# Kernel optimization log

Measured on AMD Instinct MI355X. Metric: run time of the kernel, lower is better.

The kernel has to match this reference:

```python
import jax, jax.numpy as jnp
import numpy as np

B, C1, C2, NH, HC, EC, GC, NTXT, H, W = 8, 128, 128, 4, 32, 128, 512, 32, 160, 160
GA_HEADS, GA_HD, K_NN, NUM_SELECT = 4, 32, 6, 64  # graph attn: min(nh,4) heads, head_dim=C1/4
BN_EPS = 1e-5


def setup_inputs() -> dict:
    key = jax.random.key(0)
    ks = jax.random.split(key, 16)
    rn = lambda k, shape, s=0.05: jax.random.normal(k, shape, dtype=jnp.float32) * s
    return {
        'x': jax.random.normal(ks[0], (B, C1, H, W), dtype=jnp.float32),
        'guide': jax.random.normal(ks[1], (B, NTXT, GC), dtype=jnp.float32),
        'w_gm1': rn(ks[2], (C1 // 4, C1)), 'b_gm1': jnp.zeros((C1 // 4,), jnp.float32),
        'w_gm2': rn(ks[3], (GA_HEADS, C1 // 4)), 'b_gm2': jnp.zeros((GA_HEADS,), jnp.float32),
        'w_qkv': rn(ks[4], (3 * C1, C1)),
        'w_ge1': rn(ks[5], (C1 // 2, C1)), 'b_ge1': jnp.zeros((C1 // 2,), jnp.float32),
        'w_ge2': rn(ks[6], (GA_HEADS, C1 // 2)), 'b_ge2': jnp.zeros((GA_HEADS,), jnp.float32),
        'w_gl': rn(ks[7], (EC, GC)), 'b_gl': jnp.zeros((EC,), jnp.float32),
        'attn_bias': rn(ks[8], (NH,), 0.1),
        'w_proj': rn(ks[9], (C2, C1, 3, 3)),
        'bn_gamma': jnp.ones((C2,), jnp.float32), 'bn_beta': jnp.zeros((C2,), jnp.float32),
        'bn_mean': rn(ks[10], (C2,)),
        'bn_var': jax.random.uniform(ks[11], (C2,), jnp.float32, 0.5, 1.5),
    }


def _graph_attention(x, w_gm1, b_gm1, w_gm2, b_gm2, w_qkv, w_ge1, b_ge1, w_ge2, b_ge2):
    # EfficientGraphModulatedAttention.forward (eval mode, dropout off)
    b, c, h, w = x.shape
    # spatial modulation: 1x1 conv -> relu -> 1x1 conv -> sigmoid   [B,GA_HEADS,H,W]
    h1 = jax.nn.relu(jnp.einsum('bchw,oc->bohw', x, w_gm1) + b_gm1[None, :, None, None])
    sm = jax.nn.sigmoid(jnp.einsum('bchw,oc->bohw', h1, w_gm2) + b_gm2[None, :, None, None])
    # top-k important pixels per image (num_select = min(64, int(H*W*0.005)))
    imp = jnp.abs(x).mean(axis=1).reshape(b, h * w)
    _, top_idx = jax.lax.top_k(imp, NUM_SELECT)                       # [B,S]
    x_flat = x.reshape(b, c, h * w).transpose(0, 2, 1)                # [B,HW,C]
    sel = jnp.take_along_axis(x_flat, top_idx[:, :, None], axis=1)    # [B,S,C]

    def per_sample(feats):                                            # feats: [S,C]
        s = feats.shape[0]
        # KNN graph over cosine similarity; self-edges dropped (as in torch loop)
        nf = feats / jnp.clip(jnp.linalg.norm(feats, axis=1, keepdims=True), 1e-12)
        sim = nf @ nf.T                                               # [S,S]
        _, nbr = jax.lax.top_k(sim, K_NN + 1)                         # [S,K+1]
        src = jnp.repeat(jnp.arange(s), K_NN + 1)
        dst = nbr.reshape(-1)
        valid = src != dst
        # local multi-head attention over selected nodes
        qkv = (feats @ w_qkv.T).reshape(s, 3, GA_HEADS, GA_HD).transpose(1, 2, 0, 3)
        q, k, v = qkv[0], qkv[1], qkv[2]                              # [GA_HEADS,S,GA_HD]
        scores = jnp.einsum('hse,hte->hst', q, k) * (GA_HD ** -0.5)
        # edge modulation (identical for every head in the torch code)
        gw = jax.nn.relu(feats @ w_ge1.T + b_ge1) @ w_ge2.T + b_ge2   # [S,GA_HEADS]
        ew = (gw[src] * gw[dst]).mean(axis=-1)                        # [E]
        mod = jnp.zeros((s, s), feats.dtype).at[src, dst].set(jnp.where(valid, ew, 0.0))
        attn = jax.nn.softmax(scores + 0.1 * mod[None], axis=-1)
        return attn.mean(axis=(0, 2))                                 # pixel importance [S]

    pix = jax.vmap(per_sample)(sel)                                   # [B,S]
    gmw_flat = jnp.zeros((b, h * w), x.dtype).at[jnp.arange(b)[:, None], top_idx].set(pix)
    gmw = jnp.broadcast_to(gmw_flat.reshape(b, 1, h, w), (b, GA_HEADS, h, w))
    final_mod = 0.7 * sm + 0.3 * gmw
    return x * final_mod.mean(axis=1, keepdims=True)


def _forward(x, guide, w_gm1, b_gm1, w_gm2, b_gm2, w_qkv, w_ge1, b_ge1, w_ge2, b_ge2,
             w_gl, b_gl, attn_bias, w_proj, bn_gamma, bn_beta, bn_mean, bn_var):
    bs, _, h, w = x.shape
    x_mod = _graph_attention(x, w_gm1, b_gm1, w_gm2, b_gm2, w_qkv, w_ge1, b_ge1, w_ge2, b_ge2)
    x = x + 0.1 * x_mod
    g = (guide @ w_gl.T + b_gl).reshape(bs, -1, NH, HC)               # [B,n,NH,HC]
    embed = x.reshape(bs, NH, HC, h, w)                               # self.ec is None (c1==ec)
    aw = jnp.einsum('bmchw,bnmc->bmhwn', embed, g)
    aw = aw.max(axis=-1) / np.sqrt(HC).astype(np.float32)
    aw = jax.nn.sigmoid(aw + attn_bias[None, :, None, None]) * 1.0    # scale buffer == 1
    aw_single = aw.mean(axis=1)                                       # [B,H,W]
    xp = jax.lax.conv_general_dilated(x, w_proj, (1, 1), 'SAME',
                                      dimension_numbers=('NCHW', 'OIHW', 'NCHW'))
    s = bn_gamma / jnp.sqrt(bn_var + BN_EPS)                          # eval-mode BN
    xp = xp * s[None, :, None, None] + (bn_beta - bn_mean * s)[None, :, None, None]
    xp = xp.reshape(bs, NH, HC, h, w) * aw[:, :, None]
    return xp.reshape(bs, -1, h, w), aw_single


def reference(x, guide, w_gm1, b_gm1, w_gm2, b_gm2, w_qkv, w_ge1, b_ge1, w_ge2, b_ge2,
              w_gl, b_gl, attn_bias, w_proj, bn_gamma, bn_beta, bn_mean, bn_var):
    return _forward(x, guide, w_gm1, b_gm1, w_gm2, b_gm2, w_qkv, w_ge1, b_ge1, w_ge2, b_ge2,
                    w_gl, b_gl, attn_bias, w_proj, bn_gamma, bn_beta, bn_mean, bn_var)
```

## Files before the change

### kernel.cpp

```cpp
#include <hip/hip_runtime.h>
#include <hip/hip_bf16.h>
#include <math.h>

#define B_   8
#define C1_  128
#define H_   160
#define W_   160
#define HW_  25600
#define NSEL_ 64
#define BONUS_ 4.6875e-4f

typedef __attribute__((ext_vector_type(8))) unsigned short ushort8;
typedef __attribute__((ext_vector_type(8))) short short8;
typedef __attribute__((ext_vector_type(4))) float f32x4;

#define OFF_FAC 0
#define OFF_IMP 819200
#define OFF_AW4 1638400
#define OFF_G   4915200
#define OFF_TB  5046272
#define OFF_WT  5046784
#define OFF_WPK 5636608
#define OFF_XH  5931520
#define WS_NEED_FAST 58360320ULL

__device__ __forceinline__ float sigmoidf_(float v) {
    return 1.0f / (1.0f + expf(-v));
}
__device__ __forceinline__ unsigned short f2bf(float f) {
    unsigned u = __float_as_uint(f);
    return (unsigned short)((u + 0x7fffu + ((u >> 16) & 1u)) >> 16);
}
__device__ __forceinline__ float bf2f(unsigned short h) {
    return __uint_as_float(((unsigned)h) << 16);
}

__global__ __launch_bounds__(256) void k_prep(const float* __restrict__ wp,
                                              const float* __restrict__ gamma,
                                              const float* __restrict__ beta,
                                              const float* __restrict__ mean,
                                              const float* __restrict__ var,
                                              const float* __restrict__ guide,
                                              const float* __restrict__ w_gl,
                                              const float* __restrict__ b_gl,
                                              float* __restrict__ wt,
                                              float* __restrict__ tb,
                                              unsigned short* __restrict__ wpk,
                                              float* __restrict__ g) {
    const int blk = blockIdx.x;
    const int tid = threadIdx.x;
    if (blk < 576) {
        int i = blk * 256 + tid;
        if (i < 128) {
            float s = gamma[i] * rsqrtf(var[i] + 1e-5f);
            tb[i] = beta[i] - mean[i] * s;
        }
        if (i < 147456) {
            int o = i & 127, it = i >> 7;
            float s = gamma[o] * rsqrtf(var[o] + 1e-5f);
            wt[i] = wp[o * 1152 + it] * s;
        }
    } else if (blk < 1152) {
        int idx = (blk - 576) * 256 + tid;
        if (idx < 147456) {
            int j = idx & 7, l = (idx >> 3) & 63, f = idx >> 9;
            int kstep = f >> 3, mblk = f & 7;
            int tap = kstep >> 2, icb = kstep & 3;
            int oc = mblk * 16 + (l & 15);
            int ic = icb * 32 + ((l >> 4) << 3) + j;
            float s = gamma[oc] * rsqrtf(var[oc] + 1e-5f);
            wpk[idx] = f2bf(wp[oc * 1152 + ic * 9 + tap] * s);
        }
    } else {
        __shared__ float gr[2][512];
        const int half = tid >> 7, t = tid & 127;
        const int bn = (blk - 1152) * 2 + half;
        for (int i = t; i < 512; i += 128) gr[half][i] = guide[bn * 512 + i];
        __syncthreads();
        const float4* w4 = (const float4*)(w_gl + (size_t)t * 512);
        const float4* g4 = (const float4*)gr[half];
        float acc = b_gl[t];
        for (int k = 0; k < 128; ++k) {
            float4 w = w4[k]; float4 v = g4[k];
            acc += w.x * v.x + w.y * v.y + w.z * v.z + w.w * v.w;
        }
        g[bn * 128 + t] = acc;
    }
}

__global__ __launch_bounds__(512) void k1a_convert(const float* __restrict__ x,
                                                   float* __restrict__ imp,
                                                   unsigned short* __restrict__ xh) {
    __shared__ float red[8][256];
    const int tid = threadIdx.x;
    const int l = tid & 63, g = tid >> 6;
    const int px0 = blockIdx.x * 256;
    const int b = blockIdx.y;
    const int pxl = l * 4;
    const float* xb = x + (size_t)b * C1_ * HW_ + px0 + pxl;
    unsigned short* xrb = xh + ((size_t)(b * HW_ + px0 + pxl)) * 128 + g * 16;

    float sab0 = 0.f, sab1 = 0.f, sab2 = 0.f, sab3 = 0.f;
    ushort8 v0, v1, v2, v3;
#pragma unroll
    for (int j = 0; j < 16; ++j) {
        float4 xv = *reinterpret_cast<const float4*>(xb + (size_t)(g * 16 + j) * HW_);
        sab0 += fabsf(xv.x); sab1 += fabsf(xv.y);
        sab2 += fabsf(xv.z); sab3 += fabsf(xv.w);
        const int jj = j & 7;
        v0[jj] = f2bf(xv.x); v1[jj] = f2bf(xv.y);
        v2[jj] = f2bf(xv.z); v3[jj] = f2bf(xv.w);
        if (jj == 7) {
            const int gr = j & ~7;
            *reinterpret_cast<ushort8*>(xrb + 0 * 128 + gr) = v0;
            *reinterpret_cast<ushort8*>(xrb + 1 * 128 + gr) = v1;
            *reinterpret_cast<ushort8*>(xrb + 2 * 128 + gr) = v2;
            *reinterpret_cast<ushort8*>(xrb + 3 * 128 + gr) = v3;
        }
    }
    red[g][pxl + 0] = sab0; red[g][pxl + 1] = sab1;
    red[g][pxl + 2] = sab2; red[g][pxl + 3] = sab3;
    __syncthreads();
    if (tid < 256) {
        float s = 0.f;
#pragma unroll
        for (int gg = 0; gg < 8; ++gg) s += red[gg][tid];
        imp[b * HW_ + px0 + tid] = s * (1.f / 128.f);
    }
}

__global__ __launch_bounds__(256) void k1_mod(const float* __restrict__ x,
                                              const float* __restrict__ w_gm1,
                                              const float* __restrict__ b_gm1,
                                              const float* __restrict__ w_gm2,
                                              const float* __restrict__ b_gm2,
                                              float* __restrict__ fac,
                                              float* __restrict__ imp) {
    __shared__ float4 w1t[128 * 8];
    __shared__ float  b1s[32];
    __shared__ float  w2s[128];
    __shared__ float  b2s[4];
    const int tid = threadIdx.x;
    for (int i = tid; i < 4096; i += 256) {
        int j = i >> 7, c = i & 127;
        ((float*)w1t)[c * 32 + j] = w_gm1[i];
    }
    if (tid < 32) b1s[tid] = b_gm1[tid];
    if (tid < 128) w2s[tid] = w_gm2[tid];
    if (tid < 4) b2s[tid] = b_gm2[tid];
    __syncthreads();

    const int hw0 = blockIdx.x * 512 + tid * 2;
    const int b = blockIdx.y;
    const float* xb = x + (size_t)b * C1_ * HW_ + hw0;

    float h[2][32];
#pragma unroll
    for (int j = 0; j < 32; ++j) { h[0][j] = 0.f; h[1][j] = 0.f; }
    float sab0 = 0.f, sab1 = 0.f;
    for (int c8 = 0; c8 < 16; ++c8) {
#pragma unroll
        for (int k = 0; k < 8; ++k) {
            int c = c8 * 8 + k;
            float2 xv = *reinterpret_cast<const float2*>(xb + (size_t)c * HW_);
            sab0 += fabsf(xv.x);
            sab1 += fabsf(xv.y);
            const float4* wr = &w1t[c * 8];
#pragma unroll
            for (int j4 = 0; j4 < 8; ++j4) {
                float4 w = wr[j4];
                h[0][j4 * 4 + 0] += xv.x * w.x; h[0][j4 * 4 + 1] += xv.x * w.y;
                h[0][j4 * 4 + 2] += xv.x * w.z; h[0][j4 * 4 + 3] += xv.x * w.w;
                h[1][j4 * 4 + 0] += xv.y * w.x; h[1][j4 * 4 + 1] += xv.y * w.y;
                h[1][j4 * 4 + 2] += xv.y * w.z; h[1][j4 * 4 + 3] += xv.y * w.w;
            }
        }
    }
#pragma unroll
    for (int p = 0; p < 2; ++p) {
        float fm = 0.f;
#pragma unroll
        for (int j = 0; j < 32; ++j) h[p][j] = fmaxf(h[p][j] + b1s[j], 0.f);
#pragma unroll
        for (int m = 0; m < 4; ++m) {
            float s = b2s[m];
#pragma unroll
            for (int j = 0; j < 32; ++j) s += w2s[m * 32 + j] * h[p][j];
            fm += sigmoidf_(s);
        }
        fac[b * HW_ + hw0 + p] = 1.f + 0.07f * (fm * 0.25f);
        imp[b * HW_ + hw0 + p] = (p == 0 ? sab0 : sab1) * (1.f / 128.f);
    }
}

__device__ __forceinline__ int blockReduceSum1024(int v, int* red, int tid) {
#pragma unroll
    for (int off = 32; off >= 1; off >>= 1) v += __shfl_down(v, off);
    if ((tid & 63) == 0) red[tid >> 6] = v;
    __syncthreads();
    if (tid < 64) {
        int s = (tid < 16) ? red[tid] : 0;
#pragma unroll
        for (int off = 8; off >= 1; off >>= 1) s += __shfl_down(s, off);
        if (tid == 0) red[16] = s;
    }
    __syncthreads();
    int r = red[16];
    __syncthreads();
    return r;
}

__global__ __launch_bounds__(1024) void k2_topk(const float* __restrict__ imp,
                                                float* __restrict__ fac,
                                                int mode) {
    __shared__ int red[17];
    __shared__ int claimed;
    const int tid = threadIdx.x;
    const int b = blockIdx.x;
    unsigned u[25];
#pragma unroll
    for (int i = 0; i < 25; ++i)
        u[i] = __float_as_uint(imp[b * HW_ + i * 1024 + tid]);

    unsigned cur = 0u;
    for (int bit = 30; bit >= 0; --bit) {
        unsigned cand = cur | (1u << bit);
        int c = 0;
#pragma unroll
        for (int i = 0; i < 25; ++i) c += (u[i] >= cand) ? 1 : 0;
        int tot = blockReduceSum1024(c, red, tid);
        if (tot >= NSEL_) cur = cand;
    }
    int cg = 0;
#pragma unroll
    for (int i = 0; i < 25; ++i) cg += (u[i] > cur) ? 1 : 0;
    int tot_gt = blockReduceSum1024(cg, red, tid);
    int need = NSEL_ - tot_gt;
    if (tid == 0) claimed = 0;
    __syncthreads();
#pragma unroll
    for (int i = 0; i < 25; ++i) {
        int idx = i * 1024 + tid;
        float v = 0.f;
        if (u[i] > cur) {
            v = BONUS_;
        } else if (u[i] == cur) {
            int c = atomicAdd(&claimed, 1);
            if (c < need) v = BONUS_;
        }
        if (mode) fac[b * HW_ + idx] = v;
        else if (v != 0.f) fac[b * HW_ + idx] += v;
    }
}

__global__ __launch_bounds__(256) void k4m2_scores(const unsigned short* __restrict__ xh,
                                                   const float* __restrict__ g,
                                                   const float* __restrict__ w_gm1,
                                                   const float* __restrict__ b_gm1,
                                                   const float* __restrict__ w_gm2,
                                                   const float* __restrict__ b_gm2,
                                                   const float* __restrict__ attn_bias,
                                                   float* __restrict__ fac,
                                                   float* __restrict__ aw4,
                                                   float* __restrict__ aw_single) {
    __shared__ unsigned short xs[128 * 128];
    const int tid = threadIdx.x;
    const int l = tid & 63, w = tid >> 6;
    const int px0 = blockIdx.x * 128;
    const int b = blockIdx.y;

#pragma unroll
    for (int i = 0; i < 8; ++i) {
        int idx = i * 256 + tid;
        int row = idx >> 4, gg = idx & 15;
        const char* src = (const char*)(xh + ((size_t)(b * HW_ + px0 + row)) * 128
                                        + ((gg ^ (row & 7)) * 8));
        char* dst = (char*)xs + (size_t)(i * 4096 + w * 1024);
        __builtin_amdgcn_global_load_lds((const unsigned int*)src,
                                         (unsigned int*)dst, 16, 0, 0);
    }

    const int lr = l & 15, lk = l >> 4;

    short8 afr[4][2];
#pragma unroll
    for (int m = 0; m < 4; ++m)
#pragma unroll
        for (int nb = 0; nb < 2; ++nb) {
            const float* gp = g + (size_t)b * 4096 + (nb * 16 + lr) * 128
                              + m * 32 + (lk << 3);
            float4 g0 = *reinterpret_cast<const float4*>(gp);
            float4 g1 = *reinterpret_cast<const float4*>(gp + 4);
            short8 a;
            a[0] = (short)f2bf(g0.x); a[1] = (short)f2bf(g0.y);
            a[2] = (short)f2bf(g0.z); a[3] = (short)f2bf(g0.w);
            a[4] = (short)f2bf(g1.x); a[5] = (short)f2bf(g1.y);
            a[6] = (short)f2bf(g1.z); a[7] = (short)f2bf(g1.w);
            afr[m][nb] = a;
        }

    short8 w1f[2][4];
#pragma unroll
    for (int ob = 0; ob < 2; ++ob)
#pragma unroll
        for (int kb = 0; kb < 4; ++kb) {
            const float* wp = w_gm1 + (size_t)(ob * 16 + lr) * 128 + kb * 32 + (lk << 3);
            float4 g0 = *reinterpret_cast<const float4*>(wp);
            float4 g1 = *reinterpret_cast<const float4*>(wp + 4);
            short8 a;
            a[0] = (short)f2bf(g0.x); a[1] = (short)f2bf(g0.y);
            a[2] = (short)f2bf(g0.z); a[3] = (short)f2bf(g0.w);
            a[4] = (short)f2bf(g1.x); a[5] = (short)f2bf(g1.y);
            a[6] = (short)f2bf(g1.z); a[7] = (short)f2bf(g1.w);
            w1f[ob][kb] = a;
        }

    float b1r[8], w2r[4][8];
#pragma unroll
    for (int r = 0; r < 4; ++r) {
        b1r[r] = b_gm1[lk * 4 + r];
        b1r[4 + r] = b_gm1[16 + lk * 4 + r];
    }
#pragma unroll
    for (int m = 0; m < 4; ++m)
#pragma unroll
        for (int r = 0; r < 4; ++r) {
            w2r[m][r] = w_gm2[m * 32 + lk * 4 + r];
            w2r[m][4 + r] = w_gm2[m * 32 + 16 + lk * 4 + r];
        }
    const float b20 = b_gm2[0], b21 = b_gm2[1], b22 = b_gm2[2], b23 = b_gm2[3];
    const float ab0 = attn_bias[0], ab1 = attn_bias[1];
    const float ab2 = attn_bias[2], ab3 = attn_bias[3];

    __syncthreads();

#pragma unroll
    for (int pxb = 0; pxb < 2; ++pxb) {
        const int px = (w * 2 + pxb) * 16 + lr;
        float mr[4];
        f32x4 h0{0.f, 0.f, 0.f, 0.f}, h1{0.f, 0.f, 0.f, 0.f};
#pragma unroll
        for (int m = 0; m < 4; ++m) {
            int gl = (m * 4 + lk) ^ (px & 7);
            short8 bf = *reinterpret_cast<const short8*>(xs + (size_t)px * 128 + gl * 8);
            f32x4 a0{0.f, 0.f, 0.f, 0.f}, a1{0.f, 0.f, 0.f, 0.f};
            a0 = __builtin_amdgcn_mfma_f32_16x16x32_bf16(afr[m][0], bf, a0, 0, 0, 0);
            a1 = __builtin_amdgcn_mfma_f32_16x16x32_bf16(afr[m][1], bf, a1, 0, 0, 0);
            h0 = __builtin_amdgcn_mfma_f32_16x16x32_bf16(w1f[0][m], bf, h0, 0, 0, 0);
            h1 = __builtin_amdgcn_mfma_f32_16x16x32_bf16(w1f[1][m], bf, h1, 0, 0, 0);
            float v = fmaxf(fmaxf(fmaxf(a0[0], a0[1]), fmaxf(a0[2], a0[3])),
                            fmaxf(fmaxf(a1[0], a1[1]), fmaxf(a1[2], a1[3])));
            v = fmaxf(v, __shfl_xor(v, 16));
            v = fmaxf(v, __shfl_xor(v, 32));
            mr[m] = v;
        }
        float s0 = b20, s1 = b21, s2 = b22, s3 = b23;
#pragma unroll
        for (int r = 0; r < 4; ++r) {
            float hv0 = fmaxf(h0[r] + b1r[r], 0.f);
            float hv1 = fmaxf(h1[r] + b1r[4 + r], 0.f);
            s0 += w2r[0][r] * hv0 + w2r[0][4 + r] * hv1;
            s1 += w2r[1][r] * hv0 + w2r[1][4 + r] * hv1;
            s2 += w2r[2][r] * hv0 + w2r[2][4 + r] * hv1;
            s3 += w2r[3][r] * hv0 + w2r[3][4 + r] * hv1;
        }
        s0 += __shfl_xor(s0, 16); s0 += __shfl_xor(s0, 32);
        s1 += __shfl_xor(s1, 16); s1 += __shfl_xor(s1, 32);
        s2 += __shfl_xor(s2, 16); s2 += __shfl_xor(s2, 32);
        s3 += __shfl_xor(s3, 16); s3 += __shfl_xor(s3, 32);
        float fm = sigmoidf_(s0) + sigmoidf_(s1) + sigmoidf_(s2) + sigmoidf_(s3);
        if (l < 16) {
            int hw = px0 + (w * 2 + pxb) * 16 + l;
            float bonus = fac[b * HW_ + hw];
            float fv = 1.f + 0.0175f * fm + bonus;
            fac[b * HW_ + hw] = fv;
            float sc = fv * 0.17677669529663687f;
            float a0 = sigmoidf_(mr[0] * sc + ab0);
            float a1 = sigmoidf_(mr[1] * sc + ab1);
            float a2 = sigmoidf_(mr[2] * sc + ab2);
            float a3 = sigmoidf_(mr[3] * sc + ab3);
            aw4[((size_t)(b * 4 + 0)) * HW_ + hw] = a0;
            aw4[((size_t)(b * 4 + 1)) * HW_ + hw] = a1;
            aw4[((size_t)(b * 4 + 2)) * HW_ + hw] = a2;
            aw4[((size_t)(b * 4 + 3)) * HW_ + hw] = a3;
            aw_single[b * HW_ + hw] = (a0 + a1 + a2 + a3) * 0.25f;
        }
    }
}

__global__ __launch_bounds__(256) void k4_aw(const float* __restrict__ x,
                                             const float* __restrict__ fac,
                                             const float* __restrict__ g,
                                             const float* __restrict__ attn_bias,
                                             float* __restrict__ aw4,
                                             float* __restrict__ aw_single) {
    __shared__ float gl[4096];
    __shared__ float biass[4];
    const int tid = threadIdx.x;
    const int b = blockIdx.y;
    for (int i = tid; i < 4096; i += 256) {
        int n = i >> 7, e = i & 127;
        gl[e * 32 + n] = g[b * 4096 + i];
    }
    if (tid < 4) biass[tid] = attn_bias[tid];
    __syncthreads();
    const int hw = blockIdx.x * 256 + tid;
    const float facv = fac[b * HW_ + hw];
    const float* xb = x + (size_t)b * C1_ * HW_ + hw;
    float asum = 0.f;
#pragma unroll
    for (int m = 0; m < 4; ++m) {
        float acc[32];
#pragma unroll
        for (int n = 0; n < 32; ++n) acc[n] = 0.f;
        for (int c = 0; c < 32; ++c) {
            float xv = xb[(m * 32 + c) * HW_] * facv;
            const float4* grow = (const float4*)&gl[(m * 32 + c) * 32];
#pragma unroll
            for (int n4 = 0; n4 < 8; ++n4) {
                float4 gv = grow[n4];
                acc[n4 * 4 + 0] += xv * gv.x; acc[n4 * 4 + 1] += xv * gv.y;
                acc[n4 * 4 + 2] += xv * gv.z; acc[n4 * 4 + 3] += xv * gv.w;
            }
        }
        float mxv = acc[0];
#pragma unroll
        for (int n = 1; n < 32; ++n) mxv = fmaxf(mxv, acc[n]);
        float awv = sigmoidf_(mxv * 0.17677669529663687f + biass[m]);
        aw4[((size_t)(b * 4 + m)) * HW_ + hw] = awv;
        asum += awv;
    }
    aw_single[b * HW_ + hw] = asum * 0.25f;
}

__global__ __launch_bounds__(512, 4) void k5_mfma(const unsigned short* __restrict__ xh,
                                                  const float* __restrict__ fac,
                                                  const unsigned short* __restrict__ wpk,
                                                  const float* __restrict__ tb,
                                                  const float* __restrict__ aw4,
                                                  float* __restrict__ out) {
    __shared__ unsigned short xs[180 * 17 * 8];
    const int tid = threadIdx.x;
    const int l = tid & 63, w = tid >> 6;
    const int bx0 = blockIdx.x * 16;
    const int by0 = blockIdx.y * 8;
    const int b   = blockIdx.z;

    for (int i = tid; i < 2880; i += 512) {
        int gg = i & 15, pc = i >> 4;
        int hc = pc % 18, hr = pc / 18;
        int gy = by0 - 1 + hr, gx = bx0 - 1 + hc;
        ushort8 v;
#pragma unroll
        for (int k = 0; k < 8; ++k) v[k] = 0;
        if (gy >= 0 && gy < H_ && gx >= 0 && gx < W_) {
            int hw = gy * W_ + gx;
            v = *reinterpret_cast<const ushort8*>(xh + ((size_t)b * HW_ + hw) * 128 + gg * 8);
            float fv = fac[b * HW_ + hw];
#pragma unroll
            for (int k = 0; k < 8; ++k) v[k] = f2bf(bf2f(v[k]) * fv);
        }
        *reinterpret_cast<ushort8*>(xs + (size_t)(pc * 17 + gg) * 8) = v;
    }
    __syncthreads();

    const int qo = w >> 1;
    const int phalf = w & 1;
    const int lr = l & 15, lk = l >> 4;

    f32x4 acc[2][4];
#pragma unroll
    for (int mf = 0; mf < 2; ++mf)
#pragma unroll
        for (int nf = 0; nf < 4; ++nf)
#pragma unroll
            for (int r = 0; r < 4; ++r) acc[mf][nf][r] = 0.f;

    const unsigned short* wlane = wpk + (size_t)(qo * 2) * 512 + (size_t)l * 8;
    const unsigned short* xbase = xs + (size_t)((phalf * 4 * 18 + lr) * 17 + lk) * 8;

    short8 A0[2], A1[2];
#pragma unroll
    for (int mf = 0; mf < 2; ++mf) {
        A0[mf] = *reinterpret_cast<const short8*>(wlane + mf * 512);
        A1[mf] = *reinterpret_cast<const short8*>(wlane + 4096 + mf * 512);
    }

#pragma unroll 1
    for (int tap = 0; tap < 9; ++tap) {
        const int dy = (tap >= 6) ? 2 : (tap >= 3 ? 1 : 0);
        const int dx = tap - dy * 3;
        const unsigned short* bbase = xbase + (size_t)(((dy * 18 + dx) * 17) * 8);
        const unsigned short* wpre = wlane + (size_t)(tap * 4 + 2) * 4096;
#pragma unroll
        for (int icb = 0; icb < 4; ++icb) {
            const int k = tap * 4 + icb;
            short8 A2[2];
            if (k + 2 < 36) {
#pragma unroll
                for (int mf = 0; mf < 2; ++mf)
                    A2[mf] = *reinterpret_cast<const short8*>(wpre + (size_t)icb * 4096 + mf * 512);
            }
            short8 bf[4];
#pragma unroll
            for (int nf = 0; nf < 4; ++nf)
                bf[nf] = *reinterpret_cast<const short8*>(
                    bbase + (size_t)((nf * 18 * 17 + icb * 4) * 8));
#pragma unroll
            for (int mf = 0; mf < 2; ++mf)
#pragma unroll
                for (int nf = 0; nf < 4; ++nf)
                    acc[mf][nf] = __builtin_amdgcn_mfma_f32_16x16x32_bf16(
                        A0[mf], bf[nf], acc[mf][nf], 0, 0, 0);
            if (k < 35) {
#pragma unroll
                for (int mf = 0; mf < 2; ++mf) {
                    A0[mf] = A1[mf];
                    if (k + 2 < 36) A1[mf] = A2[mf];
                }
            }
        }
    }

    const float* awb = aw4 + (size_t)b * 4 * HW_;
    float* outb = out + (size_t)b * 128 * HW_;
    const int head = qo;
#pragma unroll
    for (int mf = 0; mf < 2; ++mf) {
        const int oc0 = qo * 32 + mf * 16 + lk * 4;
#pragma unroll
        for (int nf = 0; nf < 4; ++nf) {
            int px = phalf * 64 + nf * 16 + lr;
            int hw = (by0 + (px >> 4)) * W_ + bx0 + (px & 15);
            float aw = awb[(size_t)head * HW_ + hw];
#pragma unroll
            for (int r = 0; r < 4; ++r) {
                int oc = oc0 + r;
                outb[(size_t)oc * HW_ + hw] = (acc[mf][nf][r] + tb[oc]) * aw;
            }
        }
    }
}

__global__ __launch_bounds__(256) void k5_conv(const float* __restrict__ x,
                                               const float* __restrict__ fac,
                                               const float* __restrict__ wt,
                                               const float* __restrict__ tb,
                                               const float* __restrict__ aw4,
                                               float* __restrict__ out) {
    __shared__ float ft[18][36];
    __shared__ float xs[16][18][36];
    __shared__ float wl[16][9][32];
    const int tx = threadIdx.x;
    const int ty = threadIdx.y;
    const int tid = ty * 32 + tx;
    const int bx0 = blockIdx.x * 32;
    const int by0 = blockIdx.y * 16;
    const int m = blockIdx.z & 3;
    const int b = blockIdx.z >> 2;

    for (int i = tid; i < 18 * 34; i += 256) {
        int r = i / 34, c = i - r * 34;
        int gy = by0 - 1 + r, gx = bx0 - 1 + c;
        bool in = (gy >= 0) && (gy < H_) && (gx < W_) && (gx >= 0);
        ft[r][c] = in ? fac[b * HW_ + gy * W_ + gx] : 0.f;
    }
    float acc0[32], acc1[32];
#pragma unroll
    for (int i = 0; i < 32; ++i) { acc0[i] = 0.f; acc1[i] = 0.f; }
    __syncthreads();

    for (int icc = 0; icc < 8; ++icc) {
        const int ic0 = icc * 16;
        for (int i = tid; i < 4608; i += 256) {
            int ic = i / 288; int rem = i - ic * 288;
            int tap = rem >> 5; int oc = rem & 31;
            wl[ic][tap][oc] = wt[((ic0 + ic) * 9 + tap) * 128 + m * 32 + oc];
        }
        for (int i = tid; i < 16 * 612; i += 256) {
            int ic = i / 612; int j = i - ic * 612;
            int r = j / 34; int c = j - r * 34;
            int gy = by0 - 1 + r, gx = bx0 - 1 + c;
            int gyc = min(max(gy, 0), H_ - 1), gxc = min(max(gx, 0), W_ - 1);
            xs[ic][r][c] = x[((size_t)(b * C1_ + ic0 + ic)) * HW_ + gyc * W_ + gxc] * ft[r][c];
        }
        __syncthreads();
        for (int ic = 0; ic < 16; ++ic) {
#pragma unroll
            for (int ky = 0; ky < 3; ++ky) {
#pragma unroll
                for (int kx = 0; kx < 3; ++kx) {
                    float xv0 = xs[ic][ty + ky][tx + kx];
                    float xv1 = xs[ic][ty + 8 + ky][tx + kx];
                    const float4* wp = (const float4*)&wl[ic][ky * 3 + kx][0];
#pragma unroll
                    for (int o4 = 0; o4 < 8; ++o4) {
                        float4 wv = wp[o4];
                        acc0[o4 * 4 + 0] += xv0 * wv.x; acc0[o4 * 4 + 1] += xv0 * wv.y;
                        acc0[o4 * 4 + 2] += xv0 * wv.z; acc0[o4 * 4 + 3] += xv0 * wv.w;
                        acc1[o4 * 4 + 0] += xv1 * wv.x; acc1[o4 * 4 + 1] += xv1 * wv.y;
                        acc1[o4 * 4 + 2] += xv1 * wv.z; acc1[o4 * 4 + 3] += xv1 * wv.w;
                    }
                }
            }
        }
        __syncthreads();
    }

    const int hw0 = (by0 + ty) * W_ + bx0 + tx;
    const int hw1 = (by0 + ty + 8) * W_ + bx0 + tx;
    const float aw0 = aw4[((size_t)(b * 4 + m)) * HW_ + hw0];
    const float aw1 = aw4[((size_t)(b * 4 + m)) * HW_ + hw1];
    float* ob = out + ((size_t)(b * C1_ + m * 32)) * HW_;
#pragma unroll
    for (int oc = 0; oc < 32; ++oc) {
        float t = tb[m * 32 + oc];
        ob[oc * HW_ + hw0] = (acc0[oc] + t) * aw0;
        ob[oc * HW_ + hw1] = (acc1[oc] + t) * aw1;
    }
}

extern "C" void kernel_launch(void* const* d_in, const int* in_sizes, int n_in,
                              void* d_out, int out_size, void* d_ws, size_t ws_size,
                              hipStream_t stream) {
    const float* x        = (const float*)d_in[0];
    const float* guide    = (const float*)d_in[1];
    const float* w_gm1    = (const float*)d_in[2];
    const float* b_gm1    = (const float*)d_in[3];
    const float* w_gm2    = (const float*)d_in[4];
    const float* b_gm2    = (const float*)d_in[5];
    const float* w_gl     = (const float*)d_in[11];
    const float* b_gl     = (const float*)d_in[12];
    const float* attn_bias= (const float*)d_in[13];
    const float* w_proj   = (const float*)d_in[14];
    const float* bn_gamma = (const float*)d_in[15];
    const float* bn_beta  = (const float*)d_in[16];
    const float* bn_mean  = (const float*)d_in[17];
    const float* bn_var   = (const float*)d_in[18];

    char* wsb = (char*)d_ws;
    float* fac = (float*)(wsb + OFF_FAC);
    float* imp = (float*)(wsb + OFF_IMP);
    float* aw4 = (float*)(wsb + OFF_AW4);
    float* g   = (float*)(wsb + OFF_G);
    float* tb  = (float*)(wsb + OFF_TB);
    float* wt  = (float*)(wsb + OFF_WT);
    unsigned short* wpk = (unsigned short*)(wsb + OFF_WPK);
    unsigned short* xh  = (unsigned short*)(wsb + OFF_XH);

    float* out0 = (float*)d_out;
    float* out1 = (float*)d_out + (size_t)B_ * C1_ * HW_;

    const bool fast = (ws_size >= WS_NEED_FAST);

    k_prep<<<dim3(1280), dim3(256), 0, stream>>>(w_proj, bn_gamma, bn_beta, bn_mean,
                                                 bn_var, guide, w_gl, b_gl,
                                                 wt, tb, wpk, g);
    if (fast) {
        k1a_convert<<<dim3(100, 8), dim3(512), 0, stream>>>(x, imp, xh);
        k2_topk<<<dim3(8), dim3(1024), 0, stream>>>(imp, fac, 1);
        k4m2_scores<<<dim3(200, 8), dim3(256), 0, stream>>>(xh, g, w_gm1, b_gm1,
                                                            w_gm2, b_gm2, attn_bias,
                                                            fac, aw4, out1);
        k5_mfma<<<dim3(10, 20, 8), dim3(512), 0, stream>>>(xh, fac, wpk, tb, aw4, out0);
    } else {
        k1_mod<<<dim3(50, 8), dim3(256), 0, stream>>>(x, w_gm1, b_gm1, w_gm2, b_gm2,
                                                      fac, imp);
        k2_topk<<<dim3(8), dim3(1024), 0, stream>>>(imp, fac, 0);
        k4_aw<<<dim3(100, 8), dim3(256), 0, stream>>>(x, fac, g, attn_bias, aw4, out1);
        k5_conv<<<dim3(5, 10, B_ * 4), dim3(32, 8), 0, stream>>>(x, fac, wt, tb, aw4, out0);
    }
}
```

Measured before the change: 196.6 us.

## Fuse bf16 conversion with score kernel and patch top-k pixels afterwards

Merges the fp32-to-bf16 conversion/importance kernel with the MFMA scoring kernel. The converted tile is written straight into swizzled LDS, so xh no longer has to be re-read from global memory. Top-k now runs after scoring and only recomputes fac and the attention weights for the 64 selected pixels, using per-pixel max scores parked in the output buffer as scratch. This removes one launch and one global round-trip of xh. The cost is extra scratch writes and a scattered fix-up pass inside the serial top-k kernel.

New measurement: 185.1 us. 1.06x faster.

```diff
diff --git a/kernel.cpp b/kernel.cpp
--- a/kernel.cpp
+++ b/kernel.cpp
@@ -88,44 +88,175 @@
     }
 }
 
-__global__ __launch_bounds__(512) void k1a_convert(const float* __restrict__ x,
-                                                   float* __restrict__ imp,
-                                                   unsigned short* __restrict__ xh) {
-    __shared__ float red[8][256];
+__global__ __launch_bounds__(256) void k14_fused(const float* __restrict__ x,
+                                                 const float* __restrict__ g,
+                                                 const float* __restrict__ w_gm1,
+                                                 const float* __restrict__ b_gm1,
+                                                 const float* __restrict__ w_gm2,
+                                                 const float* __restrict__ b_gm2,
+                                                 const float* __restrict__ attn_bias,
+                                                 float* __restrict__ imp,
+                                                 float* __restrict__ fac,
+                                                 float* __restrict__ aw4,
+                                                 float* __restrict__ aw_single,
+                                                 float* __restrict__ mx4,
+                                                 unsigned short* __restrict__ xh) {
+    __shared__ unsigned short xs[128 * 128];
+    __shared__ float red[8][128];
     const int tid = threadIdx.x;
-    const int l = tid & 63, g = tid >> 6;
-    const int px0 = blockIdx.x * 256;
+    const int px0 = blockIdx.x * 128;
     const int b = blockIdx.y;
-    const int pxl = l * 4;
-    const float* xb = x + (size_t)b * C1_ * HW_ + px0 + pxl;
-    unsigned short* xrb = xh + ((size_t)(b * HW_ + px0 + pxl)) * 128 + g * 16;
-
-    float sab0 = 0.f, sab1 = 0.f, sab2 = 0.f, sab3 = 0.f;
-    ushort8 v0, v1, v2, v3;
-#pragma unroll
-    for (int j = 0; j < 16; ++j) {
-        float4 xv = *reinterpret_cast<const float4*>(xb + (size_t)(g * 16 + j) * HW_);
-        sab0 += fabsf(xv.x); sab1 += fabsf(xv.y);
-        sab2 += fabsf(xv.z); sab3 += fabsf(xv.w);
-        const int jj = j & 7;
-        v0[jj] = f2bf(xv.x); v1[jj] = f2bf(xv.y);
-        v2[jj] = f2bf(xv.z); v3[jj] = f2bf(xv.w);
-        if (jj == 7) {
-            const int gr = j & ~7;
-            *reinterpret_cast<ushort8*>(xrb + 0 * 128 + gr) = v0;
-            *reinterpret_cast<ushort8*>(xrb + 1 * 128 + gr) = v1;
-            *reinterpret_cast<ushort8*>(xrb + 2 * 128 + gr) = v2;
-            *reinterpret_cast<ushort8*>(xrb + 3 * 128 + gr) = v3;
-        }
-    }
-    red[g][pxl + 0] = sab0; red[g][pxl + 1] = sab1;
-    red[g][pxl + 2] = sab2; red[g][pxl + 3] = sab3;
-    __syncthreads();
-    if (tid < 256) {
+
+    {
+        const int cg = tid >> 5, pgl = tid & 31;
+        const int pxl = pgl * 4;
+        const float* xb = x + (size_t)b * C1_ * HW_ + px0 + pxl;
+        unsigned short* xrb = xh + ((size_t)(b * HW_ + px0 + pxl)) * 128 + cg * 16;
+
+        float sab0 = 0.f, sab1 = 0.f, sab2 = 0.f, sab3 = 0.f;
+        ushort8 v0[2], v1[2], v2[2], v3[2];
+#pragma unroll
+        for (int j = 0; j < 16; ++j) {
+            float4 xv = *reinterpret_cast<const float4*>(xb + (size_t)(cg * 16 + j) * HW_);
+            sab0 += fabsf(xv.x); sab1 += fabsf(xv.y);
+            sab2 += fabsf(xv.z); sab3 += fabsf(xv.w);
+            const int q = j >> 3, jj = j & 7;
+            v0[q][jj] = f2bf(xv.x); v1[q][jj] = f2bf(xv.y);
+            v2[q][jj] = f2bf(xv.z); v3[q][jj] = f2bf(xv.w);
+        }
+#pragma unroll
+        for (int q = 0; q < 2; ++q) {
+            *reinterpret_cast<ushort8*>(xrb + 0 * 128 + q * 8) = v0[q];
+            *reinterpret_cast<ushort8*>(xrb + 1 * 128 + q * 8) = v1[q];
+            *reinterpret_cast<ushort8*>(xrb + 2 * 128 + q * 8) = v2[q];
+            *reinterpret_cast<ushort8*>(xrb + 3 * 128 + q * 8) = v3[q];
+        }
+#pragma unroll
+        for (int q = 0; q < 2; ++q) {
+            const int g2 = cg * 2 + q;
+            int s0 = g2 ^ ((pxl + 0) & 7), s1 = g2 ^ ((pxl + 1) & 7);
+            int s2 = g2 ^ ((pxl + 2) & 7), s3 = g2 ^ ((pxl + 3) & 7);
+            *reinterpret_cast<ushort8*>(xs + (size_t)((pxl + 0) * 16 + s0) * 8) = v0[q];
+            *reinterpret_cast<ushort8*>(xs + (size_t)((pxl + 1) * 16 + s1) * 8) = v1[q];
+            *reinterpret_cast<ushort8*>(xs + (size_t)((pxl + 2) * 16 + s2) * 8) = v2[q];
+            *reinterpret_cast<ushort8*>(xs + (size_t)((pxl + 3) * 16 + s3) * 8) = v3[q];
+        }
+        red[cg][pxl + 0] = sab0; red[cg][pxl + 1] = sab1;
+        red[cg][pxl + 2] = sab2; red[cg][pxl + 3] = sab3;
+    }
+    __syncthreads();
+    if (tid < 128) {
         float s = 0.f;
 #pragma unroll
         for (int gg = 0; gg < 8; ++gg) s += red[gg][tid];
         imp[b * HW_ + px0 + tid] = s * (1.f / 128.f);
+    }
+
+    const int l = tid & 63, w = tid >> 6;
+    const int lr = l & 15, lk = l >> 4;
+
+    short8 afr[4][2];
+#pragma unroll
+    for (int m = 0; m < 4; ++m)
+#pragma unroll
+        for (int nb = 0; nb < 2; ++nb) {
+            const float* gp = g + (size_t)b * 4096 + (nb * 16 + lr) * 128
+                              + m * 32 + (lk << 3);
+            float4 g0 = *reinterpret_cast<const float4*>(gp);
+            float4 g1 = *reinterpret_cast<const float4*>(gp + 4);
+            short8 a;
+            a[0] = (short)f2bf(g0.x); a[1] = (short)f2bf(g0.y);
+            a[2] = (short)f2bf(g0.z); a[3] = (short)f2bf(g0.w);
+            a[4] = (short)f2bf(g1.x); a[5] = (short)f2bf(g1.y);
+            a[6] = (short)f2bf(g1.z); a[7] = (short)f2bf(g1.w);
+            afr[m][nb] = a;
+        }
+
+    short8 w1f[2][4];
+#pragma unroll
+    for (int ob = 0; ob < 2; ++ob)
+#pragma unroll
+        for (int kb = 0; kb < 4; ++kb) {
+            const float* wp = w_gm1 + (size_t)(ob * 16 + lr) * 128 + kb * 32 + (lk << 3);
+            float4 g0 = *reinterpret_cast<const float4*>(wp);
+            float4 g1 = *reinterpret_cast<const float4*>(wp + 4);
+            short8 a;
+            a[0] = (short)f2bf(g0.x); a[1] = (short)f2bf(g0.y);
+            a[2] = (short)f2bf(g0.z); a[3] = (short)f2bf(g0.w);
+            a[4] = (short)f2bf(g1.x); a[5] = (short)f2bf(g1.y);
+            a[6] = (short)f2bf(g1.z); a[7] = (short)f2bf(g1.w);
+            w1f[ob][kb] = a;
+        }
+
+    float b1r[8], w2r[4][8];
+#pragma unroll
+    for (int r = 0; r < 4; ++r) {
+        b1r[r] = b_gm1[lk * 4 + r];
+        b1r[4 + r] = b_gm1[16 + lk * 4 + r];
+    }
+#pragma unroll
+    for (int m = 0; m < 4; ++m)
+#pragma unroll
+        for (int r = 0; r < 4; ++r) {
+            w2r[m][r] = w_gm2[m * 32 + lk * 4 + r];
+            w2r[m][4 + r] = w_gm2[m * 32 + 16 + lk * 4 + r];
+        }
+    const float b20 = b_gm2[0], b21 = b_gm2[1], b22 = b_gm2[2], b23 = b_gm2[3];
+    const float ab0 = attn_bias[0], ab1 = attn_bias[1];
+    const float ab2 = attn_bias[2], ab3 = attn_bias[3];
+
+#pragma unroll
+    for (int pxb = 0; pxb < 2; ++pxb) {
+        const int px = (w * 2 + pxb) * 16 + lr;
+        float mr[4];
+        f32x4 h0{0.f, 0.f, 0.f, 0.f}, h1{0.f, 0.f, 0.f, 0.f};
+#pragma unroll
+        for (int m = 0; m < 4; ++m) {
+            int gl = (m * 4 + lk) ^ (px & 7);
+            short8 bf = *reinterpret_cast<const short8*>(xs + (size_t)px * 128 + gl * 8);
+            f32x4 a0{0.f, 0.f, 0.f, 0.f}, a1{0.f, 0.f, 0.f, 0.f};
+            a0 = __builtin_amdgcn_mfma_f32_16x16x32_bf16(afr[m][0], bf, a0, 0, 0, 0);
+            a1 = __builtin_amdgcn_mfma_f32_16x16x32_bf16(afr[m][1], bf, a1, 0, 0, 0);
+            h0 = __builtin_amdgcn_mfma_f32_16x16x32_bf16(w1f[0][m], bf, h0, 0, 0, 0);
+            h1 = __builtin_amdgcn_mfma_f32_16x16x32_bf16(w1f[1][m], bf, h1, 0, 0, 0);
+            float v = fmaxf(fmaxf(fmaxf(a0[0], a0[1]), fmaxf(a0[2], a0[3])),
+                            fmaxf(fmaxf(a1[0], a1[1]), fmaxf(a1[2], a1[3])));
+            v = fmaxf(v, __shfl_xor(v, 16));
+            v = fmaxf(v, __shfl_xor(v, 32));
+            mr[m] = v;
+        }
+        float s0 = b20, s1 = b21, s2 = b22, s3 = b23;
+#pragma unroll
+        for (int r = 0; r < 4; ++r) {
+            float hv0 = fmaxf(h0[r] + b1r[r], 0.f);
+            float hv1 = fmaxf(h1[r] + b1r[4 + r], 0.f);
+            s0 += w2r[0][r] * hv0 + w2r[0][4 + r] * hv1;
+            s1 += w2r[1][r] * hv0 + w2r[1][4 + r] * hv1;
+            s2 += w2r[2][r] * hv0 + w2r[2][4 + r] * hv1;
+            s3 += w2r[3][r] * hv0 + w2r[3][4 + r] * hv1;
+        }
+        s0 += __shfl_xor(s0, 16); s0 += __shfl_xor(s0, 32);
+        s1 += __shfl_xor(s1, 16); s1 += __shfl_xor(s1, 32);
+        s2 += __shfl_xor(s2, 16); s2 += __shfl_xor(s2, 32);
+        s3 += __shfl_xor(s3, 16); s3 += __shfl_xor(s3, 32);
+        float fm = sigmoidf_(s0) + sigmoidf_(s1) + sigmoidf_(s2) + sigmoidf_(s3);
+        if (l < 16) {
+            int hw = px0 + (w * 2 + pxb) * 16 + l;
+            float fv = 1.f + 0.0175f * fm;
+            fac[b * HW_ + hw] = fv;
+            float4 o; o.x = mr[0]; o.y = mr[1]; o.z = mr[2]; o.w = mr[3];
+            *reinterpret_cast<float4*>(mx4 + (size_t)(b * HW_ + hw) * 4) = o;
+            float sc = fv * 0.17677669529663687f;
+            float a0 = sigmoidf_(mr[0] * sc + ab0);
+            float a1 = sigmoidf_(mr[1] * sc + ab1);
+            float a2 = sigmoidf_(mr[2] * sc + ab2);
+            float a3 = sigmoidf_(mr[3] * sc + ab3);
+            aw4[((size_t)(b * 4 + 0)) * HW_ + hw] = a0;
+            aw4[((size_t)(b * 4 + 1)) * HW_ + hw] = a1;
+            aw4[((size_t)(b * 4 + 2)) * HW_ + hw] = a2;
+            aw4[((size_t)(b * 4 + 3)) * HW_ + hw] = a3;
+            aw_single[b * HW_ + hw] = (a0 + a1 + a2 + a3) * 0.25f;
+        }
     }
 }
 
@@ -210,8 +341,35 @@
     return r;
 }
 
+__device__ __forceinline__ void bump_px2(float* __restrict__ fac,
+                                         const float* __restrict__ mx4,
+                                         float* __restrict__ aw4,
+                                         float* __restrict__ aw_single,
+                                         const float* __restrict__ attn_bias,
+                                         int b, int idx, int mode) {
+    float fv = fac[b * HW_ + idx] + BONUS_;
+    fac[b * HW_ + idx] = fv;
+    if (mode) {
+        float4 mv = *reinterpret_cast<const float4*>(mx4 + (size_t)(b * HW_ + idx) * 4);
+        float sc = fv * 0.17677669529663687f;
+        float a0 = sigmoidf_(mv.x * sc + attn_bias[0]);
+        float a1 = sigmoidf_(mv.y * sc + attn_bias[1]);
+        float a2 = sigmoidf_(mv.z * sc + attn_bias[2]);
+        float a3 = sigmoidf_(mv.w * sc + attn_bias[3]);
+        aw4[((size_t)(b * 4 + 0)) * HW_ + idx] = a0;
+        aw4[((size_t)(b * 4 + 1)) * HW_ + idx] = a1;
+        aw4[((size_t)(b * 4 + 2)) * HW_ + idx] = a2;
+        aw4[((size_t)(b * 4 + 3)) * HW_ + idx] = a3;
+        aw_single[b * HW_ + idx] = (a0 + a1 + a2 + a3) * 0.25f;
+    }
+}
+
 __global__ __launch_bounds__(1024) void k2_topk(const float* __restrict__ imp,
                                                 float* __restrict__ fac,
+                                                const float* __restrict__ mx4,
+                                                float* __restrict__ aw4,
+                                                float* __restrict__ aw_single,
+                                                const float* __restrict__ attn_bias,
                                                 int mode) {
     __shared__ int red[17];
     __shared__ int claimed;
@@ -241,149 +399,11 @@
 #pragma unroll
     for (int i = 0; i < 25; ++i) {
         int idx = i * 1024 + tid;
-        float v = 0.f;
         if (u[i] > cur) {
-            v = BONUS_;
+            bump_px2(fac, mx4, aw4, aw_single, attn_bias, b, idx, mode);
         } else if (u[i] == cur) {
             int c = atomicAdd(&claimed, 1);
-            if (c < need) v = BONUS_;
-        }
-        if (mode) fac[b * HW_ + idx] = v;
-        else if (v != 0.f) fac[b * HW_ + idx] += v;
-    }
-}
-
-__global__ __launch_bounds__(256) void k4m2_scores(const unsigned short* __restrict__ xh,
-                                                   const float* __restrict__ g,
-                                                   const float* __restrict__ w_gm1,
-                                                   const float* __restrict__ b_gm1,
-                                                   const float* __restrict__ w_gm2,
-                                                   const float* __restrict__ b_gm2,
-                                                   const float* __restrict__ attn_bias,
-                                                   float* __restrict__ fac,
-                                                   float* __restrict__ aw4,
-                                                   float* __restrict__ aw_single) {
-    __shared__ unsigned short xs[128 * 128];
-    const int tid = threadIdx.x;
-    const int l = tid & 63, w = tid >> 6;
-    const int px0 = blockIdx.x * 128;
-    const int b = blockIdx.y;
-
-#pragma unroll
-    for (int i = 0; i < 8; ++i) {
-        int idx = i * 256 + tid;
-        int row = idx >> 4, gg = idx & 15;
-        const char* src = (const char*)(xh + ((size_t)(b * HW_ + px0 + row)) * 128
-                                        + ((gg ^ (row & 7)) * 8));
-        char* dst = (char*)xs + (size_t)(i * 4096 + w * 1024);
-        __builtin_amdgcn_global_load_lds((const unsigned int*)src,
-                                         (unsigned int*)dst, 16, 0, 0);
-    }
-
-    const int lr = l & 15, lk = l >> 4;
-
-    short8 afr[4][2];
-#pragma unroll
-    for (int m = 0; m < 4; ++m)
-#pragma unroll
-        for (int nb = 0; nb < 2; ++nb) {
-            const float* gp = g + (size_t)b * 4096 + (nb * 16 + lr) * 128
-                              + m * 32 + (lk << 3);
-            float4 g0 = *reinterpret_cast<const float4*>(gp);
-            float4 g1 = *reinterpret_cast<const float4*>(gp + 4);
-            short8 a;
-            a[0] = (short)f2bf(g0.x); a[1] = (short)f2bf(g0.y);
-            a[2] = (short)f2bf(g0.z); a[3] = (short)f2bf(g0.w);
-            a[4] = (short)f2bf(g1.x); a[5] = (short)f2bf(g1.y);
-            a[6] = (short)f2bf(g1.z); a[7] = (short)f2bf(g1.w);
-            afr[m][nb] = a;
-        }
-
-    short8 w1f[2][4];
-#pragma unroll
-    for (int ob = 0; ob < 2; ++ob)
-#pragma unroll
-        for (int kb = 0; kb < 4; ++kb) {
-            const float* wp = w_gm1 + (size_t)(ob * 16 + lr) * 128 + kb * 32 + (lk << 3);
-            float4 g0 = *reinterpret_cast<const float4*>(wp);
-            float4 g1 = *reinterpret_cast<const float4*>(wp + 4);
-            short8 a;
-            a[0] = (short)f2bf(g0.x); a[1] = (short)f2bf(g0.y);
-            a[2] = (short)f2bf(g0.z); a[3] = (short)f2bf(g0.w);
-            a[4] = (short)f2bf(g1.x); a[5] = (short)f2bf(g1.y);
-            a[6] = (short)f2bf(g1.z); a[7] = (short)f2bf(g1.w);
-            w1f[ob][kb] = a;
-        }
-
-    float b1r[8], w2r[4][8];
-#pragma unroll
-    for (int r = 0; r < 4; ++r) {
-        b1r[r] = b_gm1[lk * 4 + r];
-        b1r[4 + r] = b_gm1[16 + lk * 4 + r];
-    }
-#pragma unroll
-    for (int m = 0; m < 4; ++m)
-#pragma unroll
-        for (int r = 0; r < 4; ++r) {
-            w2r[m][r] = w_gm2[m * 32 + lk * 4 + r];
-            w2r[m][4 + r] = w_gm2[m * 32 + 16 + lk * 4 + r];
-        }
-    const float b20 = b_gm2[0], b21 = b_gm2[1], b22 = b_gm2[2], b23 = b_gm2[3];
-    const float ab0 = attn_bias[0], ab1 = attn_bias[1];
-    const float ab2 = attn_bias[2], ab3 = attn_bias[3];
-
-    __syncthreads();
-
-#pragma unroll
-    for (int pxb = 0; pxb < 2; ++pxb) {
-        const int px = (w * 2 + pxb) * 16 + lr;
-        float mr[4];
-        f32x4 h0{0.f, 0.f, 0.f, 0.f}, h1{0.f, 0.f, 0.f, 0.f};
-#pragma unroll
-        for (int m = 0; m < 4; ++m) {
-            int gl = (m * 4 + lk) ^ (px & 7);
-            short8 bf = *reinterpret_cast<const short8*>(xs + (size_t)px * 128 + gl * 8);
-            f32x4 a0{0.f, 0.f, 0.f, 0.f}, a1{0.f, 0.f, 0.f, 0.f};
-            a0 = __builtin_amdgcn_mfma_f32_16x16x32_bf16(afr[m][0], bf, a0, 0, 0, 0);
-            a1 = __builtin_amdgcn_mfma_f32_16x16x32_bf16(afr[m][1], bf, a1, 0, 0, 0);
-            h0 = __builtin_amdgcn_mfma_f32_16x16x32_bf16(w1f[0][m], bf, h0, 0, 0, 0);
-            h1 = __builtin_amdgcn_mfma_f32_16x16x32_bf16(w1f[1][m], bf, h1, 0, 0, 0);
-            float v = fmaxf(fmaxf(fmaxf(a0[0], a0[1]), fmaxf(a0[2], a0[3])),
-                            fmaxf(fmaxf(a1[0], a1[1]), fmaxf(a1[2], a1[3])));
-            v = fmaxf(v, __shfl_xor(v, 16));
-            v = fmaxf(v, __shfl_xor(v, 32));
-            mr[m] = v;
-        }
-        float s0 = b20, s1 = b21, s2 = b22, s3 = b23;
-#pragma unroll
-        for (int r = 0; r < 4; ++r) {
-            float hv0 = fmaxf(h0[r] + b1r[r], 0.f);
-            float hv1 = fmaxf(h1[r] + b1r[4 + r], 0.f);
-            s0 += w2r[0][r] * hv0 + w2r[0][4 + r] * hv1;
-            s1 += w2r[1][r] * hv0 + w2r[1][4 + r] * hv1;
-            s2 += w2r[2][r] * hv0 + w2r[2][4 + r] * hv1;
-            s3 += w2r[3][r] * hv0 + w2r[3][4 + r] * hv1;
-        }
-        s0 += __shfl_xor(s0, 16); s0 += __shfl_xor(s0, 32);
-        s1 += __shfl_xor(s1, 16); s1 += __shfl_xor(s1, 32);
-        s2 += __shfl_xor(s2, 16); s2 += __shfl_xor(s2, 32);
-        s3 += __shfl_xor(s3, 16); s3 += __shfl_xor(s3, 32);
-        float fm = sigmoidf_(s0) + sigmoidf_(s1) + sigmoidf_(s2) + sigmoidf_(s3);
-        if (l < 16) {
-            int hw = px0 + (w * 2 + pxb) * 16 + l;
-            float bonus = fac[b * HW_ + hw];
-            float fv = 1.f + 0.0175f * fm + bonus;
-            fac[b * HW_ + hw] = fv;
-            float sc = fv * 0.17677669529663687f;
-            float a0 = sigmoidf_(mr[0] * sc + ab0);
-            float a1 = sigmoidf_(mr[1] * sc + ab1);
-            float a2 = sigmoidf_(mr[2] * sc + ab2);
-            float a3 = sigmoidf_(mr[3] * sc + ab3);
-            aw4[((size_t)(b * 4 + 0)) * HW_ + hw] = a0;
-            aw4[((size_t)(b * 4 + 1)) * HW_ + hw] = a1;
-            aw4[((size_t)(b * 4 + 2)) * HW_ + hw] = a2;
-            aw4[((size_t)(b * 4 + 3)) * HW_ + hw] = a3;
-            aw_single[b * HW_ + hw] = (a0 + a1 + a2 + a3) * 0.25f;
+            if (c < need) bump_px2(fac, mx4, aw4, aw_single, attn_bias, b, idx, mode);
         }
     }
 }
@@ -650,6 +670,7 @@
 
     float* out0 = (float*)d_out;
     float* out1 = (float*)d_out + (size_t)B_ * C1_ * HW_;
+    float* mx4  = (float*)d_out;
 
     const bool fast = (ws_size >= WS_NEED_FAST);
 
@@ -657,16 +678,17 @@
                                                  bn_var, guide, w_gl, b_gl,
                                                  wt, tb, wpk, g);
     if (fast) {
-        k1a_convert<<<dim3(100, 8), dim3(512), 0, stream>>>(x, imp, xh);
-        k2_topk<<<dim3(8), dim3(1024), 0, stream>>>(imp, fac, 1);
-        k4m2_scores<<<dim3(200, 8), dim3(256), 0, stream>>>(xh, g, w_gm1, b_gm1,
-                                                            w_gm2, b_gm2, attn_bias,
-                                                            fac, aw4, out1);
+        k14_fused<<<dim3(200, 8), dim3(256), 0, stream>>>(x, g, w_gm1, b_gm1,
+                                                          w_gm2, b_gm2, attn_bias,
+                                                          imp, fac, aw4, out1, mx4, xh);
+        k2_topk<<<dim3(8), dim3(1024), 0, stream>>>(imp, fac, mx4, aw4, out1,
+                                                    attn_bias, 1);
         k5_mfma<<<dim3(10, 20, 8), dim3(512), 0, stream>>>(xh, fac, wpk, tb, aw4, out0);
     } else {
         k1_mod<<<dim3(50, 8), dim3(256), 0, stream>>>(x, w_gm1, b_gm1, w_gm2, b_gm2,
                                                       fac, imp);
-        k2_topk<<<dim3(8), dim3(1024), 0, stream>>>(imp, fac, 0);
+        k2_topk<<<dim3(8), dim3(1024), 0, stream>>>(imp, fac, nullptr, nullptr, nullptr,
+                                                    attn_bias, 0);
         k4_aw<<<dim3(100, 8), dim3(256), 0, stream>>>(x, fac, g, attn_bias, aw4, out1);
         k5_conv<<<dim3(5, 10, B_ * 4), dim3(32, 8), 0, stream>>>(x, fac, wt, tb, aw4, out0);
     }
```
